# Optimization experiments

Hardware: AMD Instinct MI355X
Metric: run time of the kernel (lower is better)

## Reference

```python
import jax, jax.numpy as jnp
import numpy as np

B, S, HQ, HKV, D = 2, 1024, 32, 8, 128

def setup_inputs() -> dict:
    key = jax.random.key(0)
    k1, k2, k3 = jax.random.split(key, 3)
    xq = jax.random.normal(k1, (B, S, HQ, D), dtype=jnp.float32)
    xk = jax.random.normal(k2, (B, S, HKV, D), dtype=jnp.float32)
    xv = jax.random.normal(k3, (B, S, HKV, D), dtype=jnp.float32)
    kv_buffer = jnp.zeros((B * S, 2 * HKV, D), dtype=jnp.float32)
    cur_select_index = jnp.arange(B * S, dtype=jnp.int64 if jax.config.read('jax_enable_x64') else jnp.int32)
    return {"xq": xq, "xk": xk, "xv": xv, "kv_buffer": kv_buffer,
            "cur_select_index": cur_select_index}


def reference(xq, xk, xv, kv_buffer, cur_select_index):
    b, s, hq, d = xq.shape
    hkv = xk.shape[2]
    group = hq // hkv

    # --- KV-cache scatter write: kv_buffer[cur_select_index] = cat(k, v) ---
    combined_kv = jnp.concatenate([xk, xv], axis=2).reshape(-1, 2 * hkv, d)
    kv_buffer_new = kv_buffer.at[cur_select_index].set(combined_kv)

    # --- causal flash-style prefill attention (GQA: repeat kv heads) ---
    scale = 1.0 / np.sqrt(d).astype(np.float32)
    k = jnp.repeat(xk, group, axis=2)  # [b, s, hq, d]
    v = jnp.repeat(xv, group, axis=2)

    scores = jnp.einsum('bqhd,bkhd->bhqk', xq, k) * scale  # [b, hq, s, s]
    causal = jnp.tril(jnp.ones((s, s), dtype=bool))
    scores = jnp.where(causal[None, None], scores, jnp.finfo(scores.dtype).min)
    attn = jax.nn.softmax(scores, axis=-1)
    out = jnp.einsum('bhqk,bkhd->bqhd', attn, v)  # [b, s, hq, d]
    out = out.reshape(b, s, hq * d)
    return out, kv_buffer_new
```

## Files before the change

### kernel.cpp

```cpp
#include <hip/hip_runtime.h>
#include <math.h>

#define B_  2
#define S_  1024
#define HQ_ 32
#define HKV_ 8
#define D_  128

typedef __bf16 bf16x8 __attribute__((ext_vector_type(8)));
typedef float  floatx4 __attribute__((ext_vector_type(4)));

static __device__ __forceinline__ unsigned pack2(float hi, float lo) {
    return __builtin_amdgcn_perm(__float_as_uint(hi), __float_as_uint(lo), 0x07060302u);
}

__global__ void kv_scatter_kernel(const float* __restrict__ xk,
                                  const float* __restrict__ xv,
                                  const int* __restrict__ sel,
                                  float* __restrict__ kv_out) {
    const int total = B_ * S_ * 2 * HKV_ * D_ / 4;
    for (int g = blockIdx.x * 256 + threadIdx.x; g < total; g += gridDim.x * 256) {
        const int t      = g >> 9;
        const int within = g & 511;
        const int idx    = sel[t];
        const float4* src = (within < 256)
            ? ((const float4*)(xk + (size_t)t * (HKV_ * D_)) + within)
            : ((const float4*)(xv + (size_t)t * (HKV_ * D_)) + (within - 256));
        ((float4*)(kv_out + (size_t)idx * (2 * HKV_ * D_)))[within] = *src;
    }
}

__global__ __launch_bounds__(256, 2)
void attn_kernel(const float* __restrict__ xq, const float* __restrict__ xk,
                 const float* __restrict__ xv, float* __restrict__ out) {
    const int b    = blockIdx.z;
    const int qt   = (b == 0) ? (int)blockIdx.x : (31 - (int)blockIdx.x);
    const int hk   = blockIdx.y;
    const int tid  = threadIdx.x;
    const int wave = tid >> 6;
    const int lane = tid & 63;
    const int l15  = lane & 15;
    const int quad = lane >> 4;
    const int L    = lane & 31;
    const int hi32 = lane >> 5;
    const int h    = hk * 4 + wave;

    __shared__ __align__(16) unsigned short Kl[2][32][136];
    __shared__ __align__(16) unsigned int   Vp[2][128][16];
    __shared__ __align__(16) unsigned short Pl[4][16][40];

    bf16x8 qf[2][4];
#pragma unroll
    for (int mt = 0; mt < 2; ++mt) {
        const int row = qt * 32 + mt * 16 + l15;
        const float* qp = xq + (((size_t)(b * S_ + row)) * HQ_ + h) * D_ + quad * 8;
#pragma unroll
        for (int ks = 0; ks < 4; ++ks) {
            union { bf16x8 v; unsigned u[4]; } t2;
            const float4 f0 = *(const float4*)(qp + ks * 32);
            const float4 f1 = *(const float4*)(qp + ks * 32 + 4);
            t2.u[0] = pack2(f0.y, f0.x); t2.u[1] = pack2(f0.w, f0.z);
            t2.u[2] = pack2(f1.y, f1.x); t2.u[3] = pack2(f1.w, f1.z);
            qf[mt][ks] = t2.v;
        }
    }

    bf16x8 ones;
    { union { bf16x8 v; unsigned u[4]; } o;
      o.u[0] = o.u[1] = o.u[2] = o.u[3] = 0x3F803F80u; ones = o.v; }

    floatx4 acc[2][8];
    floatx4 lacc[2];
#pragma unroll
    for (int mt = 0; mt < 2; ++mt) {
        lacc[mt] = (floatx4){0.f, 0.f, 0.f, 0.f};
#pragma unroll
        for (int n = 0; n < 8; ++n) acc[mt][n] = (floatx4){0.f, 0.f, 0.f, 0.f};
    }

    const float scale2 = 0.12751741f;

    float4 pk[4], pv[4];
    const int keyw = wave * 2 + hi32;

    auto loads = [&](int t) {
        const size_t base = ((size_t)(b * S_ + t * 32 + keyw) * HKV_ + hk) * D_ + 4 * L;
#pragma unroll
        for (int i = 0; i < 4; ++i) {
            pk[i] = *(const float4*)(xk + base + (size_t)i * 8 * HKV_ * D_);
            pv[i] = *(const float4*)(xv + base + (size_t)i * 8 * HKV_ * D_);
        }
    };

    auto writesLDS = [&](int bi) {
#pragma unroll
        for (int i = 0; i < 4; ++i) {
            const int key = i * 8 + keyw;
            unsigned kw0 = pack2(pk[i].y, pk[i].x), kw1 = pack2(pk[i].w, pk[i].z);
            *(uint2*)&Kl[bi][key][4 * L] = make_uint2(kw0, kw1);
            unsigned D10 = pack2(pv[i].y, pv[i].x), D32 = pack2(pv[i].w, pv[i].z);
            unsigned P10 = (unsigned)__shfl_xor((int)D10, 32);
            unsigned P32 = (unsigned)__shfl_xor((int)D32, 32);
            unsigned w0 = hi32 ? __builtin_amdgcn_perm(D10, P10, 0x07060302u)
                               : __builtin_amdgcn_perm(P10, D10, 0x05040100u);
            unsigned w2 = hi32 ? __builtin_amdgcn_perm(D32, P32, 0x07060302u)
                               : __builtin_amdgcn_perm(P32, D32, 0x05040100u);
            const int col = 4 * ((i + L) & 3) + wave;
            Vp[bi][4 * L + hi32][col]     = w0;
            Vp[bi][4 * L + hi32 + 2][col] = w2;
        }
    };

    auto compute = [&](int bi, bool lastTile) {
#pragma unroll
        for (int mt = 0; mt < 2; ++mt) {
            floatx4 s0 = (floatx4){0.f, 0.f, 0.f, 0.f};
            floatx4 s1 = (floatx4){0.f, 0.f, 0.f, 0.f};
#pragma unroll
            for (int ks = 0; ks < 4; ++ks) {
                bf16x8 kb0 = *(const bf16x8*)&Kl[bi][l15][ks * 32 + quad * 8];
                bf16x8 kb1 = *(const bf16x8*)&Kl[bi][16 + l15][ks * 32 + quad * 8];
                s0 = __builtin_amdgcn_mfma_f32_16x16x32_bf16(qf[mt][ks], kb0, s0, 0, 0, 0);
                s1 = __builtin_amdgcn_mfma_f32_16x16x32_bf16(qf[mt][ks], kb1, s1, 0, 0, 0);
            }
            float p0[4], p1[4];
            if (lastTile) {
                const int rb = mt * 16 + quad * 4;
#pragma unroll
                for (int r = 0; r < 4; ++r) {
                    p0[r] = (l15      <= rb + r) ? __builtin_amdgcn_exp2f(s0[r] * scale2) : 0.f;
                    p1[r] = (l15 + 16 <= rb + r) ? __builtin_amdgcn_exp2f(s1[r] * scale2) : 0.f;
                }
            } else {
#pragma unroll
                for (int r = 0; r < 4; ++r) {
                    p0[r] = __builtin_amdgcn_exp2f(s0[r] * scale2);
                    p1[r] = __builtin_amdgcn_exp2f(s1[r] * scale2);
                }
            }
#pragma unroll
            for (int r = 0; r < 4; ++r) {
                Pl[wave][quad * 4 + r][l15]      = (unsigned short)(__float_as_uint(p0[r]) >> 16);
                Pl[wave][quad * 4 + r][16 + l15] = (unsigned short)(__float_as_uint(p1[r]) >> 16);
            }
            bf16x8 pa = *(const bf16x8*)&Pl[wave][l15][quad * 8];
            lacc[mt] = __builtin_amdgcn_mfma_f32_16x16x32_bf16(pa, ones, lacc[mt], 0, 0, 0);
#pragma unroll
            for (int n = 0; n < 8; ++n) {
                const int d  = n * 16 + l15;
                const int cb = 4 * ((quad + (d >> 2)) & 3);
                bf16x8 vb = *(const bf16x8*)&Vp[bi][d][cb];
                acc[mt][n] = __builtin_amdgcn_mfma_f32_16x16x32_bf16(pa, vb, acc[mt][n], 0, 0, 0);
            }
        }
    };

    const int nkt = qt + 1;
    loads(0);
    writesLDS(0);
    __syncthreads();
    for (int t = 0; t < nkt; ++t) {
        const int bi = t & 1;
        if (t + 1 < nkt) loads(t + 1);
        compute(bi, t == nkt - 1);
        if (t + 1 < nkt) writesLDS(1 - bi);
        __syncthreads();
    }

#pragma unroll
    for (int mt = 0; mt < 2; ++mt) {
#pragma unroll
        for (int r = 0; r < 4; ++r) {
            const float inv = __builtin_amdgcn_rcpf(lacc[mt][r]);
            const int row = qt * 32 + mt * 16 + quad * 4 + r;
            float* op = out + (((size_t)(b * S_ + row)) * HQ_ + h) * D_ + l15;
#pragma unroll
            for (int n = 0; n < 8; ++n) op[n * 16] = acc[mt][n][r] * inv;
        }
    }
}

extern "C" void kernel_launch(void* const* d_in, const int* in_sizes, int n_in,
                              void* d_out, int out_size, void* d_ws, size_t ws_size,
                              hipStream_t stream) {
    const float* xq  = (const float*)d_in[0];
    const float* xk  = (const float*)d_in[1];
    const float* xv  = (const float*)d_in[2];
    const int*   sel = (const int*)d_in[4];

    float* out    = (float*)d_out;
    float* kv_out = out + (size_t)B_ * S_ * HQ_ * D_;

    kv_scatter_kernel<<<dim3(512), dim3(256), 0, stream>>>(xk, xv, sel, kv_out);
    attn_kernel<<<dim3(32, 8, 2), dim3(256), 0, stream>>>(xq, xk, xv, out);
}
```

Before: 147.3 us.

## Halve query tile to 16 rows per wave and double grid for occupancy

```diff
diff --git a/kernel.cpp b/kernel.cpp
--- a/kernel.cpp
+++ b/kernel.cpp
@@ -30,11 +30,11 @@
     }
 }
 
-__global__ __launch_bounds__(256, 2)
+__global__ __launch_bounds__(256, 4)
 void attn_kernel(const float* __restrict__ xq, const float* __restrict__ xk,
                  const float* __restrict__ xv, float* __restrict__ out) {
     const int b    = blockIdx.z;
-    const int qt   = (b == 0) ? (int)blockIdx.x : (31 - (int)blockIdx.x);
+    const int qt   = (b == 0) ? (int)blockIdx.x : (63 - (int)blockIdx.x);
     const int hk   = blockIdx.y;
     const int tid  = threadIdx.x;
     const int wave = tid >> 6;
@@ -49,10 +49,9 @@
     __shared__ __align__(16) unsigned int   Vp[2][128][16];
     __shared__ __align__(16) unsigned short Pl[4][16][40];
 
-    bf16x8 qf[2][4];
-#pragma unroll
-    for (int mt = 0; mt < 2; ++mt) {
-        const int row = qt * 32 + mt * 16 + l15;
+    bf16x8 qf[4];
+    {
+        const int row = qt * 16 + l15;
         const float* qp = xq + (((size_t)(b * S_ + row)) * HQ_ + h) * D_ + quad * 8;
 #pragma unroll
         for (int ks = 0; ks < 4; ++ks) {
@@ -61,7 +60,7 @@
             const float4 f1 = *(const float4*)(qp + ks * 32 + 4);
             t2.u[0] = pack2(f0.y, f0.x); t2.u[1] = pack2(f0.w, f0.z);
             t2.u[2] = pack2(f1.y, f1.x); t2.u[3] = pack2(f1.w, f1.z);
-            qf[mt][ks] = t2.v;
+            qf[ks] = t2.v;
         }
     }
 
@@ -69,14 +68,10 @@
     { union { bf16x8 v; unsigned u[4]; } o;
       o.u[0] = o.u[1] = o.u[2] = o.u[3] = 0x3F803F80u; ones = o.v; }
 
-    floatx4 acc[2][8];
-    floatx4 lacc[2];
+    floatx4 acc[8];
+    floatx4 lacc = (floatx4){0.f, 0.f, 0.f, 0.f};
 #pragma unroll
-    for (int mt = 0; mt < 2; ++mt) {
-        lacc[mt] = (floatx4){0.f, 0.f, 0.f, 0.f};
-#pragma unroll
-        for (int n = 0; n < 8; ++n) acc[mt][n] = (floatx4){0.f, 0.f, 0.f, 0.f};
-    }
+    for (int n = 0; n < 8; ++n) acc[n] = (floatx4){0.f, 0.f, 0.f, 0.f};
 
     const float scale2 = 0.12751741f;
 
@@ -111,72 +106,70 @@
         }
     };
 
-    auto compute = [&](int bi, bool lastTile) {
+    auto compute = [&](int bi, int kt, bool lastTile) {
+        floatx4 s0 = (floatx4){0.f, 0.f, 0.f, 0.f};
+        floatx4 s1 = (floatx4){0.f, 0.f, 0.f, 0.f};
 #pragma unroll
-        for (int mt = 0; mt < 2; ++mt) {
-            floatx4 s0 = (floatx4){0.f, 0.f, 0.f, 0.f};
-            floatx4 s1 = (floatx4){0.f, 0.f, 0.f, 0.f};
-#pragma unroll
-            for (int ks = 0; ks < 4; ++ks) {
-                bf16x8 kb0 = *(const bf16x8*)&Kl[bi][l15][ks * 32 + quad * 8];
-                bf16x8 kb1 = *(const bf16x8*)&Kl[bi][16 + l15][ks * 32 + quad * 8];
-                s0 = __builtin_amdgcn_mfma_f32_16x16x32_bf16(qf[mt][ks], kb0, s0, 0, 0, 0);
-                s1 = __builtin_amdgcn_mfma_f32_16x16x32_bf16(qf[mt][ks], kb1, s1, 0, 0, 0);
-            }
-            float p0[4], p1[4];
-            if (lastTile) {
-                const int rb = mt * 16 + quad * 4;
-#pragma unroll
-                for (int r = 0; r < 4; ++r) {
-                    p0[r] = (l15      <= rb + r) ? __builtin_amdgcn_exp2f(s0[r] * scale2) : 0.f;
-                    p1[r] = (l15 + 16 <= rb + r) ? __builtin_amdgcn_exp2f(s1[r] * scale2) : 0.f;
-                }
-            } else {
-#pragma unroll
-                for (int r = 0; r < 4; ++r) {
-                    p0[r] = __builtin_amdgcn_exp2f(s0[r] * scale2);
-                    p1[r] = __builtin_amdgcn_exp2f(s1[r] * scale2);
-                }
-            }
+        for (int ks = 0; ks < 4; ++ks) {
+            bf16x8 kb0 = *(const bf16x8*)&Kl[bi][l15][ks * 32 + quad * 8];
+            bf16x8 kb1 = *(const bf16x8*)&Kl[bi][16 + l15][ks * 32 + quad * 8];
+            s0 = __builtin_amdgcn_mfma_f32_16x16x32_bf16(qf[ks], kb0, s0, 0, 0, 0);
+            s1 = __builtin_amdgcn_mfma_f32_16x16x32_bf16(qf[ks], kb1, s1, 0, 0, 0);
+        }
+        float p0[4], p1[4];
+        if (lastTile) {
+            const int rowg = qt * 16 + quad * 4;
+            const int key0 = kt * 32 + l15;
+            const int key1 = kt * 32 + 16 + l15;
 #pragma unroll
             for (int r = 0; r < 4; ++r) {
-                Pl[wave][quad * 4 + r][l15]      = (unsigned short)(__float_as_uint(p0[r]) >> 16);
-                Pl[wave][quad * 4 + r][16 + l15] = (unsigned short)(__float_as_uint(p1[r]) >> 16);
+                p0[r] = (key0 <= rowg + r) ? __builtin_amdgcn_exp2f(s0[r] * scale2) : 0.f;
+                p1[r] = (key1 <= rowg + r) ? __builtin_amdgcn_exp2f(s1[r] * scale2) : 0.f;
             }
-            bf16x8 pa = *(const bf16x8*)&Pl[wave][l15][quad * 8];
-            lacc[mt] = __builtin_amdgcn_mfma_f32_16x16x32_bf16(pa, ones, lacc[mt], 0, 0, 0);
+        } else {
 #pragma unroll
-            for (int n = 0; n < 8; ++n) {
-                const int d  = n * 16 + l15;
-                const int cb = 4 * ((quad + (d >> 2)) & 3);
-                bf16x8 vb = *(const bf16x8*)&Vp[bi][d][cb];
-                acc[mt][n] = __builtin_amdgcn_mfma_f32_16x16x32_bf16(pa, vb, acc[mt][n], 0, 0, 0);
+            for (int r = 0; r < 4; ++r) {
+                p0[r] = __builtin_amdgcn_exp2f(s0[r] * scale2);
+                p1[r] = __builtin_amdgcn_exp2f(s1[r] * scale2);
             }
+        }
+#pragma unroll
+        for (int r = 0; r < 4; ++r) {
+            Pl[wave][quad * 4 + r][l15]      = (unsigned short)(__float_as_uint(p0[r]) >> 16);
+            Pl[wave][quad * 4 + r][16 + l15] = (unsigned short)(__float_as_uint(p1[r]) >> 16);
+        }
+        bf16x8 pa = *(const bf16x8*)&Pl[wave][l15][quad * 8];
+        lacc = __builtin_amdgcn_mfma_f32_16x16x32_bf16(pa, ones, lacc, 0, 0, 0);
+#pragma unroll
+        for (int n = 0; n < 8; ++n) {
+            const int d  = n * 16 + l15;
+            const int cb = 4 * ((quad + (d >> 2)) & 3);
+            bf16x8 vb = *(const bf16x8*)&Vp[bi][d][cb];
+            acc[n] = __builtin_amdgcn_mfma_f32_16x16x32_bf16(pa, vb, acc[n], 0, 0, 0);
         }
     };
 
-    const int nkt = qt + 1;
+    const int nkt = qt / 2 + 1;
     loads(0);
     writesLDS(0);
     __syncthreads();
     for (int t = 0; t < nkt; ++t) {
         const int bi = t & 1;
         if (t + 1 < nkt) loads(t + 1);
-        compute(bi, t == nkt - 1);
-        if (t + 1 < nkt) writesLDS(1 - bi);
-        __syncthreads();
+        compute(bi, t, t == nkt - 1);
+        if (t + 1 < nkt) {
+            writesLDS(1 - bi);
+            __syncthreads();
+        }
     }
 
 #pragma unroll
-    for (int mt = 0; mt < 2; ++mt) {
+    for (int r = 0; r < 4; ++r) {
+        const float inv = __builtin_amdgcn_rcpf(lacc[r]);
+        const int row = qt * 16 + quad * 4 + r;
+        float* op = out + (((size_t)(b * S_ + row)) * HQ_ + h) * D_ + l15;
 #pragma unroll
-        for (int r = 0; r < 4; ++r) {
-            const float inv = __builtin_amdgcn_rcpf(lacc[mt][r]);
-            const int row = qt * 32 + mt * 16 + quad * 4 + r;
-            float* op = out + (((size_t)(b * S_ + row)) * HQ_ + h) * D_ + l15;
-#pragma unroll
-            for (int n = 0; n < 8; ++n) op[n * 16] = acc[mt][n][r] * inv;
-        }
+        for (int n = 0; n < 8; ++n) op[n * 16] = acc[n][r] * inv;
     }
 }
 
@@ -192,5 +185,5 @@
     float* kv_out = out + (size_t)B_ * S_ * HQ_ * D_;
 
     kv_scatter_kernel<<<dim3(512), dim3(256), 0, stream>>>(xk, xv, sel, kv_out);
-    attn_kernel<<<dim3(32, 8, 2), dim3(256), 0, stream>>>(xq, xk, xv, out);
+    attn_kernel<<<dim3(64, 8, 2), dim3(256), 0, stream>>>(xq, xk, xv, out);
 }
```

After: 170.9 us. +16.0%, slower.

## Switch attention to transposed 32x32x16 MFMA with register-resident P and row sums

Applied to the files above, without the earlier changes.

```diff
diff --git a/kernel.cpp b/kernel.cpp
--- a/kernel.cpp
+++ b/kernel.cpp
@@ -8,7 +8,7 @@
 #define D_  128
 
 typedef __bf16 bf16x8 __attribute__((ext_vector_type(8)));
-typedef float  floatx4 __attribute__((ext_vector_type(4)));
+typedef float  floatx16 __attribute__((ext_vector_type(16)));
 
 static __device__ __forceinline__ unsigned pack2(float hi, float lo) {
     return __builtin_amdgcn_perm(__float_as_uint(hi), __float_as_uint(lo), 0x07060302u);
@@ -39,44 +39,34 @@
     const int tid  = threadIdx.x;
     const int wave = tid >> 6;
     const int lane = tid & 63;
-    const int l15  = lane & 15;
-    const int quad = lane >> 4;
     const int L    = lane & 31;
     const int hi32 = lane >> 5;
     const int h    = hk * 4 + wave;
 
     __shared__ __align__(16) unsigned short Kl[2][32][136];
     __shared__ __align__(16) unsigned int   Vp[2][128][16];
-    __shared__ __align__(16) unsigned short Pl[4][16][40];
 
-    bf16x8 qf[2][4];
+    bf16x8 qb[8];
+    {
+        const int q = qt * 32 + L;
+        const float* qp = xq + (((size_t)(b * S_ + q)) * HQ_ + h) * D_ + 8 * hi32;
 #pragma unroll
-    for (int mt = 0; mt < 2; ++mt) {
-        const int row = qt * 32 + mt * 16 + l15;
-        const float* qp = xq + (((size_t)(b * S_ + row)) * HQ_ + h) * D_ + quad * 8;
-#pragma unroll
-        for (int ks = 0; ks < 4; ++ks) {
+        for (int s = 0; s < 8; ++s) {
             union { bf16x8 v; unsigned u[4]; } t2;
-            const float4 f0 = *(const float4*)(qp + ks * 32);
-            const float4 f1 = *(const float4*)(qp + ks * 32 + 4);
+            const float4 f0 = *(const float4*)(qp + 16 * s);
+            const float4 f1 = *(const float4*)(qp + 16 * s + 4);
             t2.u[0] = pack2(f0.y, f0.x); t2.u[1] = pack2(f0.w, f0.z);
             t2.u[2] = pack2(f1.y, f1.x); t2.u[3] = pack2(f1.w, f1.z);
-            qf[mt][ks] = t2.v;
+            qb[s] = t2.v;
         }
     }
 
-    bf16x8 ones;
-    { union { bf16x8 v; unsigned u[4]; } o;
-      o.u[0] = o.u[1] = o.u[2] = o.u[3] = 0x3F803F80u; ones = o.v; }
-
-    floatx4 acc[2][8];
-    floatx4 lacc[2];
+    floatx16 acc[4];
 #pragma unroll
-    for (int mt = 0; mt < 2; ++mt) {
-        lacc[mt] = (floatx4){0.f, 0.f, 0.f, 0.f};
+    for (int nt = 0; nt < 4; ++nt)
 #pragma unroll
-        for (int n = 0; n < 8; ++n) acc[mt][n] = (floatx4){0.f, 0.f, 0.f, 0.f};
-    }
+        for (int i = 0; i < 16; ++i) acc[nt][i] = 0.f;
+    float l_run = 0.f;
 
     const float scale2 = 0.12751741f;
 
@@ -112,46 +102,51 @@
     };
 
     auto compute = [&](int bi, bool lastTile) {
+        floatx16 sc;
 #pragma unroll
-        for (int mt = 0; mt < 2; ++mt) {
-            floatx4 s0 = (floatx4){0.f, 0.f, 0.f, 0.f};
-            floatx4 s1 = (floatx4){0.f, 0.f, 0.f, 0.f};
+        for (int i = 0; i < 16; ++i) sc[i] = 0.f;
 #pragma unroll
-            for (int ks = 0; ks < 4; ++ks) {
-                bf16x8 kb0 = *(const bf16x8*)&Kl[bi][l15][ks * 32 + quad * 8];
-                bf16x8 kb1 = *(const bf16x8*)&Kl[bi][16 + l15][ks * 32 + quad * 8];
-                s0 = __builtin_amdgcn_mfma_f32_16x16x32_bf16(qf[mt][ks], kb0, s0, 0, 0, 0);
-                s1 = __builtin_amdgcn_mfma_f32_16x16x32_bf16(qf[mt][ks], kb1, s1, 0, 0, 0);
+        for (int ks = 0; ks < 8; ++ks) {
+            bf16x8 kf = *(const bf16x8*)&Kl[bi][L][ks * 16 + 8 * hi32];
+            sc = __builtin_amdgcn_mfma_f32_32x32x16_bf16(kf, qb[ks], sc, 0, 0, 0);
+        }
+        float p[16];
+        if (lastTile) {
+#pragma unroll
+            for (int r = 0; r < 16; ++r) {
+                const int row = (r & 3) + 8 * (r >> 2) + 4 * hi32;
+                p[r] = (row <= L) ? __builtin_amdgcn_exp2f(sc[r] * scale2) : 0.f;
             }
-            float p0[4], p1[4];
-            if (lastTile) {
-                const int rb = mt * 16 + quad * 4;
+        } else {
 #pragma unroll
-                for (int r = 0; r < 4; ++r) {
-                    p0[r] = (l15      <= rb + r) ? __builtin_amdgcn_exp2f(s0[r] * scale2) : 0.f;
-                    p1[r] = (l15 + 16 <= rb + r) ? __builtin_amdgcn_exp2f(s1[r] * scale2) : 0.f;
-                }
-            } else {
+            for (int r = 0; r < 16; ++r) p[r] = __builtin_amdgcn_exp2f(sc[r] * scale2);
+        }
+        float ls = 0.f;
 #pragma unroll
-                for (int r = 0; r < 4; ++r) {
-                    p0[r] = __builtin_amdgcn_exp2f(s0[r] * scale2);
-                    p1[r] = __builtin_amdgcn_exp2f(s1[r] * scale2);
-                }
-            }
+        for (int r = 0; r < 16; ++r) ls += p[r];
+        ls += __shfl_xor(ls, 32);
+        l_run += ls;
+        unsigned Dw[8], Xw[8];
 #pragma unroll
-            for (int r = 0; r < 4; ++r) {
-                Pl[wave][quad * 4 + r][l15]      = (unsigned short)(__float_as_uint(p0[r]) >> 16);
-                Pl[wave][quad * 4 + r][16 + l15] = (unsigned short)(__float_as_uint(p1[r]) >> 16);
-            }
-            bf16x8 pa = *(const bf16x8*)&Pl[wave][l15][quad * 8];
-            lacc[mt] = __builtin_amdgcn_mfma_f32_16x16x32_bf16(pa, ones, lacc[mt], 0, 0, 0);
+        for (int g = 0; g < 4; ++g) {
+            Dw[2 * g]     = pack2(p[4 * g + 1], p[4 * g]);
+            Dw[2 * g + 1] = pack2(p[4 * g + 3], p[4 * g + 2]);
+        }
 #pragma unroll
-            for (int n = 0; n < 8; ++n) {
-                const int d  = n * 16 + l15;
-                const int cb = 4 * ((quad + (d >> 2)) & 3);
-                bf16x8 vb = *(const bf16x8*)&Vp[bi][d][cb];
-                acc[mt][n] = __builtin_amdgcn_mfma_f32_16x16x32_bf16(pa, vb, acc[mt][n], 0, 0, 0);
-            }
+        for (int j = 0; j < 8; ++j) Xw[j] = (unsigned)__shfl_xor((int)Dw[j], 32);
+        union { bf16x8 v; unsigned u[4]; } f0, f1;
+        f0.u[0] = hi32 ? Xw[2] : Dw[0];  f0.u[1] = hi32 ? Xw[3] : Dw[1];
+        f0.u[2] = hi32 ? Dw[2] : Xw[0];  f0.u[3] = hi32 ? Dw[3] : Xw[1];
+        f1.u[0] = hi32 ? Xw[6] : Dw[4];  f1.u[1] = hi32 ? Xw[7] : Dw[5];
+        f1.u[2] = hi32 ? Dw[6] : Xw[4];  f1.u[3] = hi32 ? Dw[7] : Xw[5];
+        const int rotb = (L >> 2) & 3;
+#pragma unroll
+        for (int nt = 0; nt < 4; ++nt) {
+            const int d = nt * 32 + L;
+            bf16x8 v0 = *(const bf16x8*)&Vp[bi][d][4 * ((hi32 + rotb) & 3)];
+            acc[nt] = __builtin_amdgcn_mfma_f32_32x32x16_bf16(v0, f0.v, acc[nt], 0, 0, 0);
+            bf16x8 v1 = *(const bf16x8*)&Vp[bi][d][4 * ((2 + hi32 + rotb) & 3)];
+            acc[nt] = __builtin_amdgcn_mfma_f32_32x32x16_bf16(v1, f1.v, acc[nt], 0, 0, 0);
         }
     };
 
@@ -163,21 +158,26 @@
         const int bi = t & 1;
         if (t + 1 < nkt) loads(t + 1);
         compute(bi, t == nkt - 1);
-        if (t + 1 < nkt) writesLDS(1 - bi);
-        __syncthreads();
+        if (t + 1 < nkt) {
+            writesLDS(1 - bi);
+            __syncthreads();
+        }
     }
 
+    const float inv = __builtin_amdgcn_rcpf(l_run);
+    const int q = qt * 32 + L;
+    float* op = out + (((size_t)(b * S_ + q)) * HQ_ + h) * D_;
 #pragma unroll
-    for (int mt = 0; mt < 2; ++mt) {
+    for (int nt = 0; nt < 4; ++nt)
 #pragma unroll
-        for (int r = 0; r < 4; ++r) {
-            const float inv = __builtin_amdgcn_rcpf(lacc[mt][r]);
-            const int row = qt * 32 + mt * 16 + quad * 4 + r;
-            float* op = out + (((size_t)(b * S_ + row)) * HQ_ + h) * D_ + l15;
-#pragma unroll
-            for (int n = 0; n < 8; ++n) op[n * 16] = acc[mt][n][r] * inv;
+        for (int g = 0; g < 4; ++g) {
+            float4 o4;
+            o4.x = acc[nt][4 * g + 0] * inv;
+            o4.y = acc[nt][4 * g + 1] * inv;
+            o4.z = acc[nt][4 * g + 2] * inv;
+            o4.w = acc[nt][4 * g + 3] * inv;
+            *(float4*)(op + nt * 32 + 8 * g + 4 * hi32) = o4;
         }
-    }
 }
 
 extern "C" void kernel_launch(void* const* d_in, const int* in_sizes, int n_in,
```

Result: no change. 148.0 us (+0.5%).
